# Kernel tuning notes

Measured on AMD Instinct MI355X. Metric: run time of the kernel, lower is better.

## Reference

```python
import jax, jax.numpy as jnp
import numpy as np

B, S, DM, H, HD = 2, 4096, 768, 12, 64
SCALING = HD ** -0.5
LN_EPS = 1e-12
ROPE_BASE = 10000.0


def rotate_half(x):
    x1, x2 = jnp.split(x, 2, axis=-1)
    return jnp.concatenate([-x2, x1], axis=-1)


def setup_inputs() -> dict:
    key = jax.random.key(0)
    ks = jax.random.split(key, 8)
    s = 0.02
    hidden_states = jax.random.normal(ks[0], (B, S, DM), dtype=jnp.float32)
    # true rotary tables: inv_freq over head_dim/2, duplicated (HF convention)
    inv_freq = 1.0 / (ROPE_BASE ** (jnp.arange(0, HD, 2, dtype=jnp.float32) / HD))
    freqs = jnp.arange(S, dtype=jnp.float32)[:, None] * inv_freq[None, :]  # [S, HD/2]
    emb = jnp.concatenate([freqs, freqs], axis=-1)                          # [S, HD]
    cos, sin = jnp.cos(emb), jnp.sin(emb)
    return {
        "hidden_states": hidden_states,
        "cos": cos,
        "sin": sin,
        "Wq": jax.random.normal(ks[1], (DM, DM), dtype=jnp.float32) * s,
        "bq": jnp.zeros((DM,), dtype=jnp.float32),
        "Wk": jax.random.normal(ks[2], (DM, DM), dtype=jnp.float32) * s,
        "bk": jnp.zeros((DM,), dtype=jnp.float32),
        "Wv": jax.random.normal(ks[3], (DM, DM), dtype=jnp.float32) * s,
        "bv": jnp.zeros((DM,), dtype=jnp.float32),
        "Wo": jax.random.normal(ks[4], (DM, DM), dtype=jnp.float32) * s,
        "ln_g": jnp.ones((DM,), dtype=jnp.float32),
        "ln_b": jnp.zeros((DM,), dtype=jnp.float32),
    }


def reference(hidden_states, cos, sin, Wq, bq, Wk, bk, Wv, bv, Wo, ln_g, ln_b):
    # QKV projections -> [B, H, S, HD]
    def proj(W, b):
        return (hidden_states @ W.T + b).reshape(B, S, H, HD).transpose(0, 2, 1, 3)
    q, k, v = proj(Wq, bq), proj(Wk, bk), proj(Wv, bv)

    # RoPE (cos/sin broadcast over batch & heads)
    c = cos[None, None, :, :]
    s_ = sin[None, None, :, :]
    q = q * c + rotate_half(q) * s_
    k = k * c + rotate_half(k) * s_

    # Faithful to source: q pre-scaled, then eager attention scales scores again
    q = q * SCALING
    scores = jnp.einsum("bhsd,bhtd->bhst", q, k) * SCALING  # [B,H,S,S]
    probs = jax.nn.softmax(scores.astype(jnp.float32), axis=-1).astype(v.dtype)
    attn = jnp.einsum("bhst,bhtd->bhsd", probs, v)
    attn = attn.transpose(0, 2, 1, 3).reshape(B, S, DM)

    # output dense (no bias) + residual + LayerNorm
    out = attn @ Wo.T + hidden_states
    mu = jnp.mean(out, axis=-1, keepdims=True)
    var = jnp.var(out, axis=-1, keepdims=True)
    out = (out - mu) * jax.lax.rsqrt(var + LN_EPS) * ln_g + ln_b
    return out
```

## Files before the change

### kernel.cpp

```cpp
#include <hip/hip_runtime.h>
#include <math.h>

#define B_   2
#define S_   4096
#define DM_  768
#define H_   12
#define HD_  64
#define M_   (B_ * S_)
#define ROWELEMS ((size_t)M_ * DM_)
#define WELEMS  ((size_t)DM_ * DM_)

#define QSC (1.4426950408889634f / 64.0f)

typedef unsigned short u16;
typedef unsigned int   u32;
typedef __attribute__((ext_vector_type(8))) short  short8;
typedef __attribute__((ext_vector_type(4))) float  floatx4;

__device__ inline u16 f2bf(float f) {
    u32 u = __builtin_bit_cast(u32, f);
    u += 0x7FFF + ((u >> 16) & 1);
    return (u16)(u >> 16);
}
__device__ inline float bf2f(u16 h) {
    return __builtin_bit_cast(float, (u32)h << 16);
}
__device__ inline u32 pk_trunc(float a, float b) {
    return __builtin_amdgcn_perm(__builtin_bit_cast(u32, b),
                                 __builtin_bit_cast(u32, a), 0x07060302);
}

__device__ inline int sw_off(int r, int cg) {
    return (r << 6) + ((cg ^ (r & 7)) << 3);
}

__device__ __forceinline__ void load_lds16(const u16* g, u16* l) {
    __builtin_amdgcn_global_load_lds(
        (const __attribute__((address_space(1))) u32*)g,
        (__attribute__((address_space(3))) u32*)l, 16, 0, 0);
}

__global__ __launch_bounds__(256) void conv_bf16(
    const float* __restrict__ h,  const float* __restrict__ wq,
    const float* __restrict__ wk, const float* __restrict__ wv,
    const float* __restrict__ wo, u16* __restrict__ hb, u16* __restrict__ wb)
{
    const int y = blockIdx.y;
    const float* src; u16* dst; size_t n4;
    if (y == 0)      { src = h;  dst = hb;              n4 = ROWELEMS / 4; }
    else if (y == 1) { src = wq; dst = wb;              n4 = WELEMS / 4; }
    else if (y == 2) { src = wk; dst = wb + WELEMS;     n4 = WELEMS / 4; }
    else if (y == 3) { src = wv; dst = wb + 2 * WELEMS; n4 = WELEMS / 4; }
    else             { src = wo; dst = wb + 3 * WELEMS; n4 = WELEMS / 4; }
    const size_t stride = (size_t)gridDim.x * 256;
    for (size_t i = blockIdx.x * 256 + threadIdx.x; i < n4; i += stride) {
        float4 v = *(const float4*)&src[i * 4];
        u32 p0 = (u32)f2bf(v.x) | ((u32)f2bf(v.y) << 16);
        u32 p1 = (u32)f2bf(v.z) | ((u32)f2bf(v.w) << 16);
        *(uint2*)&dst[i * 4] = make_uint2(p0, p1);
    }
}

__global__ __launch_bounds__(256, 3) void gemm_qkv(
    const u16* __restrict__ A,
    const u16* __restrict__ W0, const u16* __restrict__ W1, const u16* __restrict__ W2,
    const float* __restrict__ b0, const float* __restrict__ b1, const float* __restrict__ b2,
    const float* __restrict__ cosT, const float* __restrict__ sinT,
    u16* __restrict__ Qh, u16* __restrict__ Kh, u16* __restrict__ Vt)
{
    __shared__ __align__(16) u16 As[128 * 64];
    __shared__ __align__(16) u16 Ws[128 * 64];

    const int tid  = threadIdx.x;
    const int wave = tid >> 6, lane = tid & 63;
    const int n16  = lane & 15, quad = lane >> 4;
    const int wm   = wave >> 1, wn = wave & 1;
    const int m0   = blockIdx.y * 128, n0 = blockIdx.x * 128;
    const int z    = blockIdx.z;

    const u16* Wz = (z == 0) ? W0 : (z == 1) ? W1 : W2;
    const float* bz = (z == 0) ? b0 : (z == 1) ? b1 : b2;

    int gao[4], ldso[4];
#pragma unroll
    for (int i = 0; i < 4; i++) {
        int g = wave * 256 + i * 64 + lane;
        int r = g >> 3, cg = (g & 7) ^ (r & 7);
        gao[i]  = r * DM_ + cg * 8;
        ldso[i] = (wave * 256 + i * 64) * 8;
    }
    const u16* Ap = A  + (size_t)m0 * DM_;
    const u16* Wp = Wz + (size_t)n0 * DM_;

    floatx4 acc[4][4];
#pragma unroll
    for (int i = 0; i < 4; i++)
#pragma unroll
        for (int j = 0; j < 4; j++) acc[i][j] = (floatx4){0.f, 0.f, 0.f, 0.f};

    for (int k0 = 0; k0 < DM_; k0 += 64) {
        __syncthreads();
#pragma unroll
        for (int i = 0; i < 4; i++) {
            load_lds16(Ap + k0 + gao[i], &As[ldso[i]]);
            load_lds16(Wp + k0 + gao[i], &Ws[ldso[i]]);
        }
        __syncthreads();
#pragma unroll
        for (int ks = 0; ks < 2; ks++) {
            short8 af[4], bf[4];
#pragma unroll
            for (int t = 0; t < 4; t++) {
                af[t] = *(const short8*)&As[sw_off(wm * 64 + t * 16 + n16, ks * 4 + quad)];
                bf[t] = *(const short8*)&Ws[sw_off(wn * 64 + t * 16 + n16, ks * 4 + quad)];
            }
#pragma unroll
            for (int i = 0; i < 4; i++)
#pragma unroll
                for (int j = 0; j < 4; j++)
                    acc[i][j] = __builtin_amdgcn_mfma_f32_16x16x32_bf16(
                        af[i], bf[j], acc[i][j], 0, 0, 0);
        }
    }

    if (z == 2) {
#pragma unroll
        for (int i = 0; i < 4; i++)
#pragma unroll
            for (int j = 0; j < 4; j++) {
                const int col = n0 + wn * 64 + j * 16 + n16;
                const int h = col >> 6, hd = col & 63;
                const int row0 = m0 + wm * 64 + i * 16 + quad * 4;
                const int b = row0 >> 12, s0 = row0 & 4095;
                const float bias = bz[col];
                float v0 = acc[i][j][0] + bias, v1 = acc[i][j][1] + bias;
                float v2 = acc[i][j][2] + bias, v3 = acc[i][j][3] + bias;
                u32 w0 = (u32)f2bf(v0) | ((u32)f2bf(v1) << 16);
                u32 w1 = (u32)f2bf(v2) | ((u32)f2bf(v3) << 16);
                *(uint2*)&Vt[((size_t)(b * H_ + h) * HD_ + hd) * S_ + s0] = make_uint2(w0, w1);
            }
    } else {
        u16* Out = (z == 0) ? Qh : Kh;
        const float sc_ = (z == 0) ? QSC : 1.0f;
#pragma unroll
        for (int i = 0; i < 4; i++)
#pragma unroll
            for (int j = 0; j < 2; j++) {
                const int col1 = n0 + wn * 64 + j * 16 + n16;
                const int col2 = col1 + 32;
                const int h = col1 >> 6, hd1 = col1 & 63;
                const float bias1 = bz[col1], bias2 = bz[col2];
#pragma unroll
                for (int r = 0; r < 4; r++) {
                    const int row = m0 + wm * 64 + i * 16 + quad * 4 + r;
                    const int b = row >> 12, s = row & 4095;
                    const float c  = cosT[s * HD_ + hd1];
                    const float sn = sinT[s * HD_ + hd1];
                    const float x1 = acc[i][j][r] + bias1;
                    const float x2 = acc[i][j + 2][r] + bias2;
                    u16* dst = Out + ((size_t)(b * H_ + h) * S_ + s) * HD_;
                    dst[hd1]      = f2bf((x1 * c - x2 * sn) * sc_);
                    dst[hd1 + 32] = f2bf((x2 * c + x1 * sn) * sc_);
                }
            }
    }
}

__global__ __launch_bounds__(256, 3) void flash_mfma(
    const u16* __restrict__ Qh, const u16* __restrict__ Kh,
    const u16* __restrict__ Vt, u16* __restrict__ O1, u16* __restrict__ O2,
    float* __restrict__ l1, float* __restrict__ l2)
{
    __shared__ __align__(16) u16 Ks[2][64 * 64];
    __shared__ __align__(16) u16 Vs[2][64 * 64];
    __shared__ __align__(16) u16 Ps[128 * 64];

    const int tid  = threadIdx.x;
    const int wave = tid >> 6, lane = tid & 63;
    const int n16  = lane & 15, quad = lane >> 4;
    const int qt   = blockIdx.x;
    const int bh   = blockIdx.y;
    const int z    = blockIdx.z;
    const size_t qk_base = (size_t)bh * S_ * HD_;
    const size_t vt_base = (size_t)bh * HD_ * S_;
    const int q0   = qt * 128;
    const int wrow = wave * 32;

    short8 qf[2][2];
#pragma unroll
    for (int rt = 0; rt < 2; rt++)
#pragma unroll
        for (int ks = 0; ks < 2; ks++)
            qf[rt][ks] = *(const short8*)&Qh[qk_base +
                (size_t)(q0 + wrow + rt * 16 + n16) * HD_ + ks * 32 + quad * 8];

    short8 ones;
#pragma unroll
    for (int j = 0; j < 8; j++) ones[j] = (short)0x3F80;

    int gk_off[2], gv_off[2], ldso[2];
#pragma unroll
    for (int i = 0; i < 2; i++) {
        int g = wave * 128 + i * 64 + lane;
        int r = g >> 3, cg = (g & 7) ^ (r & 7);
        gk_off[i] = r * HD_ + cg * 8;
        gv_off[i] = r * S_  + cg * 8;
        ldso[i]   = (wave * 128 + i * 64) * 8;
    }

    floatx4 o_acc[2][4];
    floatx4 o_l[2];
#pragma unroll
    for (int rt = 0; rt < 2; rt++) {
        o_l[rt] = (floatx4){0.f, 0.f, 0.f, 0.f};
#pragma unroll
        for (int dt = 0; dt < 4; dt++) o_acc[rt][dt] = (floatx4){0.f, 0.f, 0.f, 0.f};
    }

    const u16* Kg0 = Kh + qk_base + (size_t)(z * 32) * 64 * HD_;
    const u16* Vg0 = Vt + vt_base + (size_t)(z * 32) * 64;

#pragma unroll
    for (int i = 0; i < 2; i++) {
        load_lds16(Kg0 + gk_off[i], &Ks[0][ldso[i]]);
        load_lds16(Vg0 + gv_off[i], &Vs[0][ldso[i]]);
    }

    for (int kt = 0; kt < 32; kt++) {
        const int cur = kt & 1, nxt = cur ^ 1;
        __syncthreads();

        {
            const int ktn = (kt < 31) ? kt + 1 : 31;
            const u16* Kg = Kg0 + (size_t)ktn * 64 * HD_;
            const u16* Vg = Vg0 + (size_t)ktn * 64;
#pragma unroll
            for (int i = 0; i < 2; i++) {
                load_lds16(Kg + gk_off[i], &Ks[nxt][ldso[i]]);
                load_lds16(Vg + gv_off[i], &Vs[nxt][ldso[i]]);
            }
        }
        __builtin_amdgcn_s_waitcnt(0x0F74);

        floatx4 sct[4][2];
#pragma unroll
        for (int ct = 0; ct < 4; ct++)
#pragma unroll
            for (int rt = 0; rt < 2; rt++)
                sct[ct][rt] = (floatx4){0.f, 0.f, 0.f, 0.f};
#pragma unroll
        for (int ks = 0; ks < 2; ks++) {
            short8 kf[4];
#pragma unroll
            for (int ct = 0; ct < 4; ct++)
                kf[ct] = *(const short8*)&Ks[cur][sw_off(ct * 16 + n16, ks * 4 + quad)];
#pragma unroll
            for (int ct = 0; ct < 4; ct++)
#pragma unroll
                for (int rt = 0; rt < 2; rt++)
                    sct[ct][rt] = __builtin_amdgcn_mfma_f32_16x16x32_bf16(
                        kf[ct], qf[rt][ks], sct[ct][rt], 0, 0, 0);
        }

#pragma unroll
        for (int rt = 0; rt < 2; rt++)
#pragma unroll
            for (int ct = 0; ct < 4; ct++) {
                float p0 = __builtin_amdgcn_exp2f(sct[ct][rt][0]);
                float p1 = __builtin_amdgcn_exp2f(sct[ct][rt][1]);
                float p2 = __builtin_amdgcn_exp2f(sct[ct][rt][2]);
                float p3 = __builtin_amdgcn_exp2f(sct[ct][rt][3]);
                uint2 w = make_uint2(pk_trunc(p0, p1), pk_trunc(p2, p3));
                const int row = wrow + rt * 16 + n16;
                const int off = sw_off(row, ct * 2 + (quad >> 1)) + (quad & 1) * 4;
                *(uint2*)&Ps[off] = w;
            }

#pragma unroll
        for (int ks = 0; ks < 2; ks++) {
            short8 pa[2];
#pragma unroll
            for (int rt = 0; rt < 2; rt++)
                pa[rt] = *(const short8*)&Ps[sw_off(wrow + rt * 16 + n16, ks * 4 + quad)];
            short8 vb[4];
#pragma unroll
            for (int dt = 0; dt < 4; dt++)
                vb[dt] = *(const short8*)&Vs[cur][sw_off(dt * 16 + n16, ks * 4 + quad)];
#pragma unroll
            for (int rt = 0; rt < 2; rt++) {
#pragma unroll
                for (int dt = 0; dt < 4; dt++)
                    o_acc[rt][dt] = __builtin_amdgcn_mfma_f32_16x16x32_bf16(
                        pa[rt], vb[dt], o_acc[rt][dt], 0, 0, 0);
                o_l[rt] = __builtin_amdgcn_mfma_f32_16x16x32_bf16(
                    pa[rt], ones, o_l[rt], 0, 0, 0);
            }
        }
    }

    float* lz = z ? l2 : l1;
    if (n16 == 0) {
#pragma unroll
        for (int rt = 0; rt < 2; rt++)
#pragma unroll
            for (int r = 0; r < 4; r++)
                lz[(size_t)bh * S_ + q0 + wrow + rt * 16 + quad * 4 + r] = o_l[rt][r];
    }
    const int b = bh / H_, h = bh % H_;
    u16* Oz = z ? O2 : O1;
#pragma unroll
    for (int rt = 0; rt < 2; rt++)
#pragma unroll
        for (int r = 0; r < 4; r++) {
            const int srow = q0 + wrow + rt * 16 + quad * 4 + r;
            u16* Orow = Oz + ((size_t)b * S_ + srow) * DM_ + h * HD_;
#pragma unroll
            for (int dt = 0; dt < 4; dt++)
                Orow[dt * 16 + n16] = f2bf(o_acc[rt][dt][r]);
        }
}

__global__ __launch_bounds__(256, 4) void gemm_out(
    const u16* __restrict__ O1, const u16* __restrict__ O2,
    const float* __restrict__ l1, const float* __restrict__ l2,
    const u16* __restrict__ W, const float* __restrict__ resid,
    float* __restrict__ Cf)
{
    __shared__ __align__(16) u16 As[64 * 64];
    __shared__ __align__(16) u16 Ws[128 * 64];

    const int tid  = threadIdx.x;
    const int wave = tid >> 6, lane = tid & 63;
    const int n16  = lane & 15, quad = lane >> 4;
    const int wm   = wave >> 1, wn = wave & 1;
    const int m0   = blockIdx.y * 64, n0 = blockIdx.x * 128;

    int gwo[4], ldswo[4];
#pragma unroll
    for (int i = 0; i < 4; i++) {
        int g = wave * 256 + i * 64 + lane;
        int r = g >> 3, cg = (g & 7) ^ (r & 7);
        gwo[i]   = r * DM_ + cg * 8;
        ldswo[i] = (wave * 256 + i * 64) * 8;
    }
    const u16* Wp = W + (size_t)n0 * DM_;

    floatx4 acc[2][4];
#pragma unroll
    for (int i = 0; i < 2; i++)
#pragma unroll
        for (int j = 0; j < 4; j++) acc[i][j] = (floatx4){0.f, 0.f, 0.f, 0.f};

    for (int k0 = 0; k0 < DM_; k0 += 64) {
        __syncthreads();
#pragma unroll
        for (int i = 0; i < 4; i++)
            load_lds16(Wp + k0 + gwo[i], &Ws[ldswo[i]]);

#pragma unroll
        for (int i = 0; i < 2; i++) {
            const int ga = tid + i * 256;
            const int ra = ga >> 3, cga = ga & 7;
            const int row = m0 + ra;
            const int col0 = k0 + cga * 8;
            const int b = row >> 12, s = row & 4095, h = col0 >> 6;
            const size_t lidx = ((size_t)(b * H_ + h)) * S_ + s;
            const float inv = __builtin_amdgcn_rcpf(l1[lidx] + l2[lidx]);
            const size_t go = (size_t)row * DM_ + col0;
            uint4 a = *(const uint4*)&O1[go];
            uint4 c = *(const uint4*)&O2[go];
            u32 res[4];
#pragma unroll
            for (int w = 0; w < 4; w++) {
                u32 ua = (&a.x)[w], uc = (&c.x)[w];
                float x0 = bf2f((u16)(ua & 0xFFFF)) + bf2f((u16)(uc & 0xFFFF));
                float x1 = bf2f((u16)(ua >> 16))    + bf2f((u16)(uc >> 16));
                res[w] = (u32)f2bf(x0 * inv) | ((u32)f2bf(x1 * inv) << 16);
            }
            *(uint4*)&As[sw_off(ra, cga)] = make_uint4(res[0], res[1], res[2], res[3]);
        }
        __syncthreads();

#pragma unroll
        for (int ks = 0; ks < 2; ks++) {
            short8 af[2], bf[4];
#pragma unroll
            for (int rt = 0; rt < 2; rt++)
                af[rt] = *(const short8*)&As[sw_off(wm * 32 + rt * 16 + n16, ks * 4 + quad)];
#pragma unroll
            for (int ct = 0; ct < 4; ct++)
                bf[ct] = *(const short8*)&Ws[sw_off(wn * 64 + ct * 16 + n16, ks * 4 + quad)];
#pragma unroll
            for (int rt = 0; rt < 2; rt++)
#pragma unroll
                for (int ct = 0; ct < 4; ct++)
                    acc[rt][ct] = __builtin_amdgcn_mfma_f32_16x16x32_bf16(
                        af[rt], bf[ct], acc[rt][ct], 0, 0, 0);
        }
    }

#pragma unroll
    for (int rt = 0; rt < 2; rt++)
#pragma unroll
        for (int ct = 0; ct < 4; ct++) {
            const int col = n0 + wn * 64 + ct * 16 + n16;
#pragma unroll
            for (int r = 0; r < 4; r++) {
                const int row = m0 + wm * 32 + rt * 16 + quad * 4 + r;
                Cf[(size_t)row * DM_ + col] = acc[rt][ct][r] + resid[(size_t)row * DM_ + col];
            }
        }
}

__global__ __launch_bounds__(256) void ln_kernel(
    float* __restrict__ io, const float* __restrict__ g, const float* __restrict__ bb)
{
    const int row = blockIdx.x, t = threadIdx.x;
    float* p = io + (size_t)row * DM_;
    float x[3];
    float sum = 0.0f, sq = 0.0f;
#pragma unroll
    for (int i = 0; i < 3; i++) {
        x[i] = p[t + i * 256];
        sum += x[i];
        sq  = fmaf(x[i], x[i], sq);
    }
#pragma unroll
    for (int off = 32; off >= 1; off >>= 1) {
        sum += __shfl_xor(sum, off);
        sq  += __shfl_xor(sq, off);
    }
    __shared__ float s1[4], s2[4];
    if ((t & 63) == 0) { s1[t >> 6] = sum; s2[t >> 6] = sq; }
    __syncthreads();
    sum = s1[0] + s1[1] + s1[2] + s1[3];
    sq  = s2[0] + s2[1] + s2[2] + s2[3];
    const float mu  = sum * (1.0f / 768.0f);
    const float var = sq * (1.0f / 768.0f) - mu * mu;
    const float rs  = rsqrtf(var + 1e-12f);
#pragma unroll
    for (int i = 0; i < 3; i++) {
        const int c = t + i * 256;
        p[c] = (x[i] - mu) * rs * g[c] + bb[c];
    }
}

extern "C" void kernel_launch(void* const* d_in, const int* in_sizes, int n_in,
                              void* d_out, int out_size, void* d_ws, size_t ws_size,
                              hipStream_t stream)
{
    const float* hidden = (const float*)d_in[0];
    const float* cosT   = (const float*)d_in[1];
    const float* sinT   = (const float*)d_in[2];
    const float* Wq     = (const float*)d_in[3];
    const float* bq     = (const float*)d_in[4];
    const float* Wk     = (const float*)d_in[5];
    const float* bk     = (const float*)d_in[6];
    const float* Wv     = (const float*)d_in[7];
    const float* bv     = (const float*)d_in[8];
    const float* Wo     = (const float*)d_in[9];
    const float* ln_g   = (const float*)d_in[10];
    const float* ln_b   = (const float*)d_in[11];
    float* out = (float*)d_out;

    u16* wsb = (u16*)d_ws;
    u16* Hb  = wsb;
    u16* Wb  = wsb + ROWELEMS;
    u16* Qh  = Wb + 4 * WELEMS;
    u16* Kh  = Qh + ROWELEMS;
    u16* Vt  = Kh + ROWELEMS;
    u16* O2  = Vt + ROWELEMS;
    float* l1 = (float*)(O2 + ROWELEMS);
    float* l2 = l1 + (size_t)B_ * H_ * S_;
    u16* O1  = Hb;
    u16* Wqb = Wb, *Wkb = Wb + WELEMS, *Wvb = Wb + 2 * WELEMS, *Wob = Wb + 3 * WELEMS;

    conv_bf16<<<dim3(1024, 5), 256, 0, stream>>>(hidden, Wq, Wk, Wv, Wo, Hb, Wb);

    gemm_qkv<<<dim3(DM_ / 128, M_ / 128, 3), 256, 0, stream>>>(
        Hb, Wqb, Wkb, Wvb, bq, bk, bv, cosT, sinT, Qh, Kh, Vt);

    flash_mfma<<<dim3(S_ / 128, B_ * H_, 2), 256, 0, stream>>>(
        Qh, Kh, Vt, O1, O2, l1, l2);

    gemm_out<<<dim3(DM_ / 128, M_ / 64), 256, 0, stream>>>(
        O1, O2, l1, l2, Wob, hidden, out);

    ln_kernel<<<M_, 256, 0, stream>>>(out, ln_g, ln_b);
}
```

Baseline: 299.0 us.

## Load K/V fragments directly from global memory, dropping LDS double buffering

Removes the shared-memory double-buffered K and V tiles and the per-iteration block barrier. Each wave now loads its K and V MFMA fragments straight from global memory into registers. This cuts LDS traffic and the sync, and frees LDS for occupancy. The cost is that every wave fetches the same K/V data separately, so global/L2 traffic rises fourfold, and load latency is no longer hidden by prefetch.

```diff
diff --git a/kernel.cpp b/kernel.cpp
--- a/kernel.cpp
+++ b/kernel.cpp
@@ -171,8 +171,6 @@
     const u16* __restrict__ Vt, u16* __restrict__ O1, u16* __restrict__ O2,
     float* __restrict__ l1, float* __restrict__ l2)
 {
-    __shared__ __align__(16) u16 Ks[2][64 * 64];
-    __shared__ __align__(16) u16 Vs[2][64 * 64];
     __shared__ __align__(16) u16 Ps[128 * 64];
 
     const int tid  = threadIdx.x;
@@ -198,16 +196,6 @@
 #pragma unroll
     for (int j = 0; j < 8; j++) ones[j] = (short)0x3F80;
 
-    int gk_off[2], gv_off[2], ldso[2];
-#pragma unroll
-    for (int i = 0; i < 2; i++) {
-        int g = wave * 128 + i * 64 + lane;
-        int r = g >> 3, cg = (g & 7) ^ (r & 7);
-        gk_off[i] = r * HD_ + cg * 8;
-        gv_off[i] = r * S_  + cg * 8;
-        ldso[i]   = (wave * 128 + i * 64) * 8;
-    }
-
     floatx4 o_acc[2][4];
     floatx4 o_l[2];
 #pragma unroll
@@ -217,30 +205,24 @@
         for (int dt = 0; dt < 4; dt++) o_acc[rt][dt] = (floatx4){0.f, 0.f, 0.f, 0.f};
     }
 
-    const u16* Kg0 = Kh + qk_base + (size_t)(z * 32) * 64 * HD_;
-    const u16* Vg0 = Vt + vt_base + (size_t)(z * 32) * 64;
-
-#pragma unroll
-    for (int i = 0; i < 2; i++) {
-        load_lds16(Kg0 + gk_off[i], &Ks[0][ldso[i]]);
-        load_lds16(Vg0 + gv_off[i], &Vs[0][ldso[i]]);
-    }
+    const u16* Kg = Kh + qk_base + (size_t)(z * 2048) * HD_
+                  + (size_t)n16 * HD_ + quad * 8;
+    const u16* Vg = Vt + vt_base + (size_t)(z * 2048)
+                  + (size_t)n16 * S_ + quad * 8;
 
     for (int kt = 0; kt < 32; kt++) {
-        const int cur = kt & 1, nxt = cur ^ 1;
-        __syncthreads();
-
-        {
-            const int ktn = (kt < 31) ? kt + 1 : 31;
-            const u16* Kg = Kg0 + (size_t)ktn * 64 * HD_;
-            const u16* Vg = Vg0 + (size_t)ktn * 64;
-#pragma unroll
-            for (int i = 0; i < 2; i++) {
-                load_lds16(Kg + gk_off[i], &Ks[nxt][ldso[i]]);
-                load_lds16(Vg + gv_off[i], &Vs[nxt][ldso[i]]);
-            }
-        }
-        __builtin_amdgcn_s_waitcnt(0x0F74);
+        short8 kf[2][4];
+#pragma unroll
+        for (int ks = 0; ks < 2; ks++)
+#pragma unroll
+            for (int ct = 0; ct < 4; ct++)
+                kf[ks][ct] = *(const short8*)&Kg[(size_t)(kt * 64 + ct * 16) * HD_ + ks * 32];
+        short8 vb[2][4];
+#pragma unroll
+        for (int ks = 0; ks < 2; ks++)
+#pragma unroll
+            for (int dt = 0; dt < 4; dt++)
+                vb[ks][dt] = *(const short8*)&Vg[(size_t)(dt * 16) * S_ + kt * 64 + ks * 32];
 
         floatx4 sct[4][2];
 #pragma unroll
@@ -249,18 +231,13 @@
             for (int rt = 0; rt < 2; rt++)
                 sct[ct][rt] = (floatx4){0.f, 0.f, 0.f, 0.f};
 #pragma unroll
-        for (int ks = 0; ks < 2; ks++) {
-            short8 kf[4];
-#pragma unroll
-            for (int ct = 0; ct < 4; ct++)
-                kf[ct] = *(const short8*)&Ks[cur][sw_off(ct * 16 + n16, ks * 4 + quad)];
+        for (int ks = 0; ks < 2; ks++)
 #pragma unroll
             for (int ct = 0; ct < 4; ct++)
 #pragma unroll
                 for (int rt = 0; rt < 2; rt++)
                     sct[ct][rt] = __builtin_amdgcn_mfma_f32_16x16x32_bf16(
-                        kf[ct], qf[rt][ks], sct[ct][rt], 0, 0, 0);
-        }
+                        kf[ks][ct], qf[rt][ks], sct[ct][rt], 0, 0, 0);
 
 #pragma unroll
         for (int rt = 0; rt < 2; rt++)
@@ -282,16 +259,12 @@
 #pragma unroll
             for (int rt = 0; rt < 2; rt++)
                 pa[rt] = *(const short8*)&Ps[sw_off(wrow + rt * 16 + n16, ks * 4 + quad)];
-            short8 vb[4];
-#pragma unroll
-            for (int dt = 0; dt < 4; dt++)
-                vb[dt] = *(const short8*)&Vs[cur][sw_off(dt * 16 + n16, ks * 4 + quad)];
 #pragma unroll
             for (int rt = 0; rt < 2; rt++) {
 #pragma unroll
                 for (int dt = 0; dt < 4; dt++)
                     o_acc[rt][dt] = __builtin_amdgcn_mfma_f32_16x16x32_bf16(
-                        pa[rt], vb[dt], o_acc[rt][dt], 0, 0, 0);
+                        pa[rt], vb[ks][dt], o_acc[rt][dt], 0, 0, 0);
                 o_l[rt] = __builtin_amdgcn_mfma_f32_16x16x32_bf16(
                     pa[rt], ones, o_l[rt], 0, 0, 0);
             }
```

Measured after the change: 525.3 us. 1.76x slower.
